# Kernel optimization log

Hardware: AMD Instinct MI355X
Metric: run time of the kernel (lower is better)

Reference implementation:

```python
import jax, jax.numpy as jnp
import numpy as np

B, H, W, CIN, COUT = 4, 128, 128, 16, 16
FH, FW = 2 * H - 1, 2 * W - 1  # fft_shape = 2*k - 1 per spatial dim (SAME, stride 1)


def setup_inputs() -> dict:
    key = jax.random.key(0)
    k1, k2, k3, k4 = jax.random.split(key, 4)
    inputs = jax.random.normal(k1, (B, H, W, CIN), dtype=jnp.float32)
    # Fourier-space complex kernel, represented as two real arrays
    kernel_real = jax.random.normal(k2, (FH, FW, CIN, COUT), dtype=jnp.float32) * 0.05
    kernel_imag = jax.random.normal(k3, (FH, FW, CIN, COUT), dtype=jnp.float32) * 0.05
    bias = jax.random.normal(k4, (1, 1, 1, COUT), dtype=jnp.float32) * 0.01
    return {"inputs": inputs, "kernel_real": kernel_real, "kernel_imag": kernel_imag, "bias": bias}


def reference(inputs, kernel_real, kernel_imag, bias):
    kernel = kernel_real + 1j * kernel_imag  # (FH, FW, CIN, COUT) complex64
    b, h, w, cin = inputs.shape
    fft_shape = (2 * h - 1, 2 * w - 1)
    # FFT over spatial dims, zero-padded to fft_shape -> (B, FH, FW, CIN) complex64
    y = jnp.fft.fftn(inputs, axes=(1, 2), s=fft_shape)
    # Broadcast complex multiply + inverse FFT: (B, FH, FW, CIN, COUT)
    y = jnp.fft.ifftn(y[..., None] * kernel, axes=(1, 2)).real
    # 'SAME' slice: center crop back to the input spatial size
    sh = (fft_shape[0] - h) // 2
    sw = (fft_shape[1] - w) // 2
    y = y[:, sh:sh + h, sw:sw + w]  # (B, H, W, CIN, COUT)
    # Faithful to the source: sum over axis=-1 (the `features` axis), leaving CIN channels
    y = jnp.sum(y, axis=-1)  # (B, H, W, CIN)
    return y + bias  # bias broadcasts because COUT == CIN
```

## Files before the change

kernel.cpp:

```cpp
#include <hip/hip_runtime.h>
#include <math.h>


constexpr float PI2_OVER_N = 6.28318530717958647692f / 255.0f;
constexpr float INV_N2 = 1.0f / (255.0f * 255.0f);

typedef __attribute__((ext_vector_type(8))) short bf16x8;
typedef __attribute__((ext_vector_type(4))) float f32x4;
#define MFMA16 __builtin_amdgcn_mfma_f32_16x16x32_bf16

__device__ __forceinline__ int remap_bc(int xidx) {
  int k = xidx & 7, j = xidx >> 3;
  return ((k >> 1) * 16) + ((k & 1) * 8) + j;
}

__device__ __forceinline__ unsigned short bf16h(float f) {
  unsigned u = __float_as_uint(f);
  return (unsigned short)((u + 0x7FFFu + ((u >> 16) & 1u)) >> 16);
}
__device__ __forceinline__ float bf16f(unsigned short h) {
  return __uint_as_float(((unsigned)h) << 16);
}


__device__ __forceinline__ void ksum_body(
    int buf, int xb, const float* __restrict__ kr, const float* __restrict__ ki,
    float* __restrict__ Sr, float* __restrict__ Si) {
  const int nrows = 255 * 255 * 16;
  int r = xb * 256 + threadIdx.x;
  if (r >= nrows) return;
  const float* src = (buf == 0) ? kr : ki;
  float* dst = (buf == 0) ? Sr : Si;
  const float4* k4 = (const float4*)(src + (size_t)r * 16);
  float4 a = k4[0], b = k4[1], c = k4[2], d = k4[3];
  dst[r] = a.x + a.y + a.z + a.w + b.x + b.y + b.z + b.w +
           c.x + c.y + c.z + c.w + d.x + d.y + d.z + d.w;
}

__device__ __forceinline__ void packx_body(
    int pid, const float* __restrict__ x, short* __restrict__ xp) {
  int bc = pid & 63;
  int mt = pid >> 6;
  int b = bc >> 4, c = bc & 15;
  int mcol = threadIdx.x & 15;
  int noct = threadIdx.x >> 4;
  int m = mt * 16 + mcol;
  const float* xs = x + ((size_t)(b * 128 + m) * 128 + noct * 8) * 16 + c;
  unsigned short hi[8], lo[8];
#pragma unroll
  for (int j = 0; j < 8; ++j) {
    float v = xs[j * 16];
    hi[j] = bf16h(v);
    lo[j] = bf16h(v - bf16f(hi[j]));
  }
  size_t base = (size_t)bc * 32768 + ((size_t)(mt * 16 + noct) * 16 + mcol) * 8;
  uint4 o;
  o.x = (unsigned)hi[0] | ((unsigned)hi[1] << 16);
  o.y = (unsigned)hi[2] | ((unsigned)hi[3] << 16);
  o.z = (unsigned)hi[4] | ((unsigned)hi[5] << 16);
  o.w = (unsigned)hi[6] | ((unsigned)hi[7] << 16);
  *(uint4*)(xp + base) = o;
  o.x = (unsigned)lo[0] | ((unsigned)lo[1] << 16);
  o.y = (unsigned)lo[2] | ((unsigned)lo[3] << 16);
  o.z = (unsigned)lo[4] | ((unsigned)lo[5] << 16);
  o.w = (unsigned)lo[6] | ((unsigned)lo[7] << 16);
  *(uint4*)(xp + base + 16384) = o;
}

__device__ __forceinline__ void buildt1_body(int cid, short* __restrict__ t1) {
  int i = cid * 256 + threadIdx.x;
  int plane = i >> 14;
  int r = i & 16383;
  int qt = r >> 11, noct = (r >> 7) & 15, qcol = (r >> 3) & 15, j = r & 7;
  int q = qt * 16 + qcol, n = noct * 8 + j;
  float s, c;
  sincosf(PI2_OVER_N * (float)((q * n) % 255), &s, &c);
  float src = (plane < 2) ? c : -s;
  unsigned short hh = bf16h(src);
  t1[i] = (short)((plane & 1) ? bf16h(src - bf16f(hh)) : hh);
}

__device__ __forceinline__ void buildt24_body(
    int cid2, short* __restrict__ t2, short* __restrict__ t4, short* __restrict__ t5) {
  int i = cid2 * 256 + threadIdx.x;
  float s, c;
  if (i < 196608) {
    int plane = i >> 15;
    int r = i & 32767;
    int pt = r >> 11, r2 = r & 2047;
    int moct = r2 >> 7, p = (r2 >> 3) & 15, j = r2 & 7;
    int pg = pt * 16 + p, m = moct * 8 + j;
    int k = ((pg % 255) * m) % 255;
    sincosf(PI2_OVER_N * (float)k, &s, &c);
    float ti = -s;
    float src = (plane < 2) ? c : ((plane < 4) ? ti : -ti);
    unsigned short h = bf16h(src);
    t2[i] = (short)((plane & 1) ? bf16h(src - bf16f(h)) : h);
  } else if (i < 393216) {
    int i2 = i - 196608;
    int plane = i2 >> 15;
    int r = i2 & 32767;
    int ht = r >> 12, r2 = r & 4095;
    int poct = r2 >> 7, h = (r2 >> 3) & 15, j = r2 & 7;
    int p = poct * 8 + j;
    unsigned short val = 0;
    if (p < 255) {
      int hg = ht * 16 + h;
      int k = ((hg + 63) * p) % 255;
      sincosf(PI2_OVER_N * (float)k, &s, &c);
      float src = (plane < 2) ? c : ((plane < 4) ? s : -s);
      unsigned short hh = bf16h(src);
      val = (plane & 1) ? bf16h(src - bf16f(hh)) : hh;
    }
    t4[i2] = (short)val;
  } else {
    int i3 = i - 393216;
    int plane = i3 >> 15;
    int r = i3 & 32767;
    int wt = r >> 12, r2 = r & 4095;
    int ko = r2 >> 7, wl = (r2 >> 3) & 15, j = r2 & 7;
    int q = (ko * 8 + j) & 127;
    int ww = wt * 16 + wl;
    sincosf(PI2_OVER_N * (float)(((ww + 63) * q) % 255), &s, &c);
    float src = (plane < 2) ? c : -s;
    unsigned short hh = bf16h(src);
    t5[i3] = (short)((plane & 1) ? bf16h(src - bf16f(hh)) : hh);
  }
}

__global__ __launch_bounds__(256) void fused_front(
    const float* __restrict__ kr, const float* __restrict__ ki,
    float* __restrict__ Sr, float* __restrict__ Si,
    const float* __restrict__ x, short* __restrict__ xp,
    short* __restrict__ t1, short* __restrict__ t2,
    short* __restrict__ t4, short* __restrict__ t5) {
  int bid = blockIdx.x;
  int d = bid >> 2, r = bid & 3;
  if (r == 3) {
    if (d < 512)      packx_body(d, x, xp);
    else if (d < 768) buildt1_body(d - 512, t1);
    else              buildt24_body(d - 768, t2, t4, t5);
  } else {
    int kid = d * 3 + r;
    if (kid < 8192) ksum_body(kid & 1, kid >> 1, kr, ki, Sr, Si);
  }
}


__device__ __forceinline__ void fold_body(
    int fid, const float* __restrict__ Sr, const float* __restrict__ Si,
    float2* __restrict__ keff2) {
  int p = fid % 255;
  int qy = fid / 255;
  int q = qy * 16 + (threadIdx.x >> 4);
  int c = threadIdx.x & 15;
  int pp = (255 - p) % 255;
  int qq = (255 - q) % 255;
  size_t i0 = (size_t)(p * 255 + q) * 16 + c;
  size_t i1 = (size_t)(pp * 255 + qq) * 16 + c;
  float sr0 = Sr[i0], si0 = Si[i0], sr1 = Sr[i1], si1 = Si[i1];
  float2 v;
  v.x = 0.5f * (sr0 + sr1);
  v.y = 0.5f * (si0 - si1);
  keff2[((size_t)c * 255 + p) * 128 + q] = v;
}

__device__ __forceinline__ void s1g_body(
    int gid, const short* __restrict__ xp, const short* __restrict__ t1,
    short* __restrict__ ub) {
  int bc = gid & 63;
  int mt = gid >> 6;
  int w = threadIdx.x >> 6;
  int lane = threadIdx.x & 63;
  int quad = lane >> 4, col = lane & 15;
  f32x4 ur[2] = {{0,0,0,0},{0,0,0,0}};
  f32x4 ui[2] = {{0,0,0,0},{0,0,0,0}};
  const short* xb = xp + (size_t)bc * 32768;
#pragma unroll
  for (int ko = 0; ko < 4; ++ko) {
    int noct = ko * 4 + quad;
    const short* pa = xb + ((size_t)(mt * 16 + noct) * 16 + col) * 8;
    bf16x8 xh = *(const bf16x8*)(pa);
    bf16x8 xl = *(const bf16x8*)(pa + 16384);
#pragma unroll
    for (int qq = 0; qq < 2; ++qq) {
      int qt = w * 2 + qq;
      const short* pb = t1 + ((size_t)(qt * 16 + noct) * 16 + col) * 8;
      bf16x8 ch = *(const bf16x8*)(pb);
      bf16x8 cl = *(const bf16x8*)(pb + 16384);
      bf16x8 nh = *(const bf16x8*)(pb + 2 * 16384);
      bf16x8 nl = *(const bf16x8*)(pb + 3 * 16384);
      ur[qq] = MFMA16(xh, ch, ur[qq], 0, 0, 0);
      ur[qq] = MFMA16(xh, cl, ur[qq], 0, 0, 0);
      ur[qq] = MFMA16(xl, ch, ur[qq], 0, 0, 0);
      ur[qq] = MFMA16(xl, cl, ur[qq], 0, 0, 0);
      ui[qq] = MFMA16(xh, nh, ui[qq], 0, 0, 0);
      ui[qq] = MFMA16(xh, nl, ui[qq], 0, 0, 0);
      ui[qq] = MFMA16(xl, nh, ui[qq], 0, 0, 0);
      ui[qq] = MFMA16(xl, nl, ui[qq], 0, 0, 0);
    }
  }
  int moct = mt * 2 + (quad >> 1);
  int j0 = (quad & 1) * 4;
#pragma unroll
  for (int qq = 0; qq < 2; ++qq) {
    int qt = w * 2 + qq;
    unsigned short rh[4], rl[4], ih[4], il[4];
#pragma unroll
    for (int r = 0; r < 4; ++r) {
      rh[r] = bf16h(ur[qq][r]); rl[r] = bf16h(ur[qq][r] - bf16f(rh[r]));
      ih[r] = bf16h(ui[qq][r]); il[r] = bf16h(ui[qq][r] - bf16f(ih[r]));
    }
    size_t base = (size_t)bc * 65536 + (size_t)qt * 2048 + (size_t)moct * 128 +
                  (size_t)col * 8 + j0;
    uint2 o;
    o.x = (unsigned)rh[0] | ((unsigned)rh[1] << 16);
    o.y = (unsigned)rh[2] | ((unsigned)rh[3] << 16);
    *(uint2*)(ub + base) = o;
    o.x = (unsigned)rl[0] | ((unsigned)rl[1] << 16);
    o.y = (unsigned)rl[2] | ((unsigned)rl[3] << 16);
    *(uint2*)(ub + base + 16384) = o;
    o.x = (unsigned)ih[0] | ((unsigned)ih[1] << 16);
    o.y = (unsigned)ih[2] | ((unsigned)ih[3] << 16);
    *(uint2*)(ub + base + 2 * 16384) = o;
    o.x = (unsigned)il[0] | ((unsigned)il[1] << 16);
    o.y = (unsigned)il[2] | ((unsigned)il[3] << 16);
    *(uint2*)(ub + base + 3 * 16384) = o;
  }
}

__global__ __launch_bounds__(256) void mid(
    const float* __restrict__ Sr, const float* __restrict__ Si,
    float2* __restrict__ keff2,
    const short* __restrict__ xp, const short* __restrict__ t1,
    short* __restrict__ ub) {
  int bid = blockIdx.x;
  int d = bid / 5, r = bid - d * 5;
  if (r == 4) {
    s1g_body(d, xp, t1, ub);
  } else {
    int fid = d * 4 + r;
    if (fid < 2040) fold_body(fid, Sr, Si, keff2);
  }
}

__global__ __launch_bounds__(256) void stage2_mfma(
    const short* __restrict__ ub, const short* __restrict__ t2,
    const float2* __restrict__ keff2, short* __restrict__ zb) {
  int bc = remap_bc(blockIdx.x);
  int c = bc & 15;
  int w = threadIdx.x >> 6;
  int lane = threadIdx.x & 63;
  int quad = lane >> 4, col = lane & 15;
  int pt = blockIdx.y;
  int qh = w;
  f32x4 accr[2] = {{0,0,0,0},{0,0,0,0}};
  f32x4 acci[2] = {{0,0,0,0},{0,0,0,0}};
  const short* ubase = ub + (size_t)bc * 65536;
#pragma unroll
  for (int ko = 0; ko < 4; ++ko) {
    int moct = ko * 4 + quad;
    const short* ta = t2 + ((size_t)(pt * 16 + moct) * 16 + col) * 8;
    bf16x8 arh = *(const bf16x8*)(ta);
    bf16x8 arl = *(const bf16x8*)(ta + 32768);
    bf16x8 aih = *(const bf16x8*)(ta + 2 * 32768);
    bf16x8 ail = *(const bf16x8*)(ta + 3 * 32768);
    bf16x8 anh = *(const bf16x8*)(ta + 4 * 32768);
    bf16x8 anl = *(const bf16x8*)(ta + 5 * 32768);
#pragma unroll
    for (int qq = 0; qq < 2; ++qq) {
      int qt = qh * 2 + qq;
      const short* tb = ubase + ((size_t)(qt * 16 + moct) * 16 + col) * 8;
      bf16x8 brh = *(const bf16x8*)(tb);
      bf16x8 brl = *(const bf16x8*)(tb + 16384);
      bf16x8 bih = *(const bf16x8*)(tb + 2 * 16384);
      bf16x8 bil = *(const bf16x8*)(tb + 3 * 16384);
      accr[qq] = MFMA16(arh, brh, accr[qq], 0, 0, 0);
      accr[qq] = MFMA16(arh, brl, accr[qq], 0, 0, 0);
      accr[qq] = MFMA16(arl, brh, accr[qq], 0, 0, 0);
      accr[qq] = MFMA16(anh, bih, accr[qq], 0, 0, 0);
      accr[qq] = MFMA16(anh, bil, accr[qq], 0, 0, 0);
      accr[qq] = MFMA16(anl, bih, accr[qq], 0, 0, 0);
      acci[qq] = MFMA16(arh, bih, acci[qq], 0, 0, 0);
      acci[qq] = MFMA16(arh, bil, acci[qq], 0, 0, 0);
      acci[qq] = MFMA16(arl, bih, acci[qq], 0, 0, 0);
      acci[qq] = MFMA16(aih, brh, acci[qq], 0, 0, 0);
      acci[qq] = MFMA16(aih, brl, acci[qq], 0, 0, 0);
      acci[qq] = MFMA16(ail, brh, acci[qq], 0, 0, 0);
    }
  }
  int poct = pt * 2 + (quad >> 1);
  size_t joff = (size_t)col * 8 + (quad & 1) * 4;
#pragma unroll
  for (int qq = 0; qq < 2; ++qq) {
    int qt = qh * 2 + qq;
    int qg = qt * 16 + col;
    float zr[4], zi[4];
#pragma unroll
    for (int r = 0; r < 4; ++r) {
      int pg = pt * 16 + quad * 4 + r;
      int pgc = pg < 255 ? pg : 254;
      float2 k = keff2[((size_t)c * 255 + pgc) * 128 + qg];
      float xr = accr[qq][r], xi = acci[qq][r];
      zr[r] = k.x * xr - k.y * xi;
      zi[r] = k.x * xi + k.y * xr;
    }
    unsigned short hr[4], lr[4], hi_[4], li[4];
#pragma unroll
    for (int r = 0; r < 4; ++r) {
      hr[r] = bf16h(zr[r]);  lr[r] = bf16h(zr[r] - bf16f(hr[r]));
      hi_[r] = bf16h(zi[r]); li[r] = bf16h(zi[r] - bf16f(hi_[r]));
    }
    size_t base = (size_t)bc * 131072 + (size_t)qt * 4096 + (size_t)poct * 128 + joff;
    uint2 o;
    o.x = (unsigned)hr[0] | ((unsigned)hr[1] << 16);
    o.y = (unsigned)hr[2] | ((unsigned)hr[3] << 16);
    *(uint2*)(zb + base) = o;
    o.x = (unsigned)lr[0] | ((unsigned)lr[1] << 16);
    o.y = (unsigned)lr[2] | ((unsigned)lr[3] << 16);
    *(uint2*)(zb + base + 32768) = o;
    o.x = (unsigned)hi_[0] | ((unsigned)hi_[1] << 16);
    o.y = (unsigned)hi_[2] | ((unsigned)hi_[3] << 16);
    *(uint2*)(zb + base + 2 * 32768) = o;
    o.x = (unsigned)li[0] | ((unsigned)li[1] << 16);
    o.y = (unsigned)li[2] | ((unsigned)li[3] << 16);
    *(uint2*)(zb + base + 3 * 32768) = o;
  }
}

__global__ __launch_bounds__(256) void stage4_mfma(
    const short* __restrict__ zb, const short* __restrict__ t4,
    short* __restrict__ a5, float* __restrict__ v0) {
  int bc = remap_bc(blockIdx.x);
  int w = threadIdx.x >> 6;
  int lane = threadIdx.x & 63;
  int quad = lane >> 4, col = lane & 15;
  int u = blockIdx.y * 4 + w;
  int qt = u >> 3;
  int kseg = (u >> 2) & 1;
  int htp = u & 3;
  f32x4 accr[2] = {{0,0,0,0},{0,0,0,0}};
  f32x4 acci[2] = {{0,0,0,0},{0,0,0,0}};
  const short* zbase = zb + (size_t)bc * 131072;
#pragma unroll
  for (int ko = 0; ko < 4; ++ko) {
    int poct = kseg * 16 + ko * 4 + quad;
    const short* tz = zbase + ((size_t)(qt * 32 + poct) * 16 + col) * 8;
    bf16x8 zrh = *(const bf16x8*)(tz);
    bf16x8 zrl = *(const bf16x8*)(tz + 32768);
    bf16x8 zih = *(const bf16x8*)(tz + 2 * 32768);
    bf16x8 zil = *(const bf16x8*)(tz + 3 * 32768);
#pragma unroll
    for (int t = 0; t < 2; ++t) {
      int ht = htp * 2 + t;
      const short* ta = t4 + ((size_t)(ht * 32 + poct) * 16 + col) * 8;
      bf16x8 trh = *(const bf16x8*)(ta);
      bf16x8 trl = *(const bf16x8*)(ta + 32768);
      bf16x8 tih = *(const bf16x8*)(ta + 2 * 32768);
      bf16x8 til = *(const bf16x8*)(ta + 3 * 32768);
      bf16x8 tnh = *(const bf16x8*)(ta + 4 * 32768);
      bf16x8 tnl = *(const bf16x8*)(ta + 5 * 32768);
      accr[t] = MFMA16(zrh, trh, accr[t], 0, 0, 0);
      accr[t] = MFMA16(zrh, trl, accr[t], 0, 0, 0);
      accr[t] = MFMA16(zrl, trh, accr[t], 0, 0, 0);
      accr[t] = MFMA16(zih, tnh, accr[t], 0, 0, 0);
      accr[t] = MFMA16(zih, tnl, accr[t], 0, 0, 0);
      accr[t] = MFMA16(zil, tnh, accr[t], 0, 0, 0);
      acci[t] = MFMA16(zih, trh, acci[t], 0, 0, 0);
      acci[t] = MFMA16(zih, trl, acci[t], 0, 0, 0);
      acci[t] = MFMA16(zil, trh, acci[t], 0, 0, 0);
      acci[t] = MFMA16(zrh, tih, acci[t], 0, 0, 0);
      acci[t] = MFMA16(zrh, til, acci[t], 0, 0, 0);
      acci[t] = MFMA16(zrl, tih, acci[t], 0, 0, 0);
    }
  }
  int ko_s = kseg * 16 + qt * 2 + (quad >> 1);
  int j0 = (quad & 1) * 4;
#pragma unroll
  for (int t = 0; t < 2; ++t) {
    int ht = htp * 2 + t;
    unsigned short vh[4], vl[4], wh[4], wl2[4];
#pragma unroll
    for (int r = 0; r < 4; ++r) {
      vh[r] = bf16h(accr[t][r]);  vl[r] = bf16h(accr[t][r] - bf16f(vh[r]));
      wh[r] = bf16h(acci[t][r]);  wl2[r] = bf16h(acci[t][r] - bf16f(wh[r]));
    }
    size_t base = (((size_t)(bc * 4) * 8 + ht) * 32 + ko_s) * 128 + (size_t)col * 8 + j0;
    uint2 o;
    o.x = (unsigned)vh[0] | ((unsigned)vh[1] << 16);
    o.y = (unsigned)vh[2] | ((unsigned)vh[3] << 16);
    *(uint2*)(a5 + base) = o;
    o.x = (unsigned)vl[0] | ((unsigned)vl[1] << 16);
    o.y = (unsigned)vl[2] | ((unsigned)vl[3] << 16);
    *(uint2*)(a5 + base + 32768) = o;
    o.x = (unsigned)wh[0] | ((unsigned)wh[1] << 16);
    o.y = (unsigned)wh[2] | ((unsigned)wh[3] << 16);
    *(uint2*)(a5 + base + 2 * 32768) = o;
    o.x = (unsigned)wl2[0] | ((unsigned)wl2[1] << 16);
    o.y = (unsigned)wl2[2] | ((unsigned)wl2[3] << 16);
    *(uint2*)(a5 + base + 3 * 32768) = o;
    if (qt == 0 && quad == 0)
      v0[(size_t)(kseg * 64 + bc) * 128 + ht * 16 + col] = accr[t][0];
  }
}

__global__ __launch_bounds__(256) void stage5_mfma(
    const short* __restrict__ a5, const short* __restrict__ t5,
    const float* __restrict__ v0, const float* __restrict__ bias,
    float* __restrict__ out) {
  int bc = remap_bc(blockIdx.x);
  int w = threadIdx.x >> 6;
  int lane = threadIdx.x & 63;
  int quad = lane >> 4, col = lane & 15;
  int u = blockIdx.y * 4 + w;
  int ht = u >> 2;
  int wtp = u & 3;
  f32x4 acc[2] = {{0,0,0,0},{0,0,0,0}};
  const short* abase = a5 + (size_t)bc * 131072;
#pragma unroll
  for (int kc = 0; kc < 8; ++kc) {
    int koq = kc * 4 + quad;
    const short* pa = abase + ((size_t)(ht * 32 + koq) * 16 + col) * 8;
    bf16x8 vrh = *(const bf16x8*)(pa);
    bf16x8 vrl = *(const bf16x8*)(pa + 32768);
    bf16x8 vih = *(const bf16x8*)(pa + 2 * 32768);
    bf16x8 vil = *(const bf16x8*)(pa + 3 * 32768);
#pragma unroll
    for (int t = 0; t < 2; ++t) {
      int wt = wtp * 2 + t;
      const short* pb = t5 + ((size_t)(wt * 32 + koq) * 16 + col) * 8;
      bf16x8 tch = *(const bf16x8*)(pb);
      bf16x8 tcl = *(const bf16x8*)(pb + 32768);
      bf16x8 tnh = *(const bf16x8*)(pb + 2 * 32768);
      bf16x8 tnl = *(const bf16x8*)(pb + 3 * 32768);
      acc[t] = MFMA16(vrh, tch, acc[t], 0, 0, 0);
      acc[t] = MFMA16(vrh, tcl, acc[t], 0, 0, 0);
      acc[t] = MFMA16(vrl, tch, acc[t], 0, 0, 0);
      acc[t] = MFMA16(vih, tnh, acc[t], 0, 0, 0);
      acc[t] = MFMA16(vih, tnl, acc[t], 0, 0, 0);
      acc[t] = MFMA16(vil, tnh, acc[t], 0, 0, 0);
    }
  }
  int b = bc >> 4, c = bc & 15;
  float bb = bias[c];
  float v0t[4];
#pragma unroll
  for (int r = 0; r < 4; ++r) {
    int h = ht * 16 + quad * 4 + r;
    v0t[r] = v0[(size_t)bc * 128 + h] + v0[(size_t)(64 + bc) * 128 + h];
  }
#pragma unroll
  for (int t = 0; t < 2; ++t) {
    int ww = (wtp * 2 + t) * 16 + col;
#pragma unroll
    for (int r = 0; r < 4; ++r) {
      int h = ht * 16 + quad * 4 + r;
      out[((size_t)(b * 128 + h) * 128 + ww) * 16 + c] =
          (2.0f * acc[t][r] - v0t[r]) * INV_N2 + bb;
    }
  }
}

extern "C" void kernel_launch(void* const* d_in, const int* in_sizes, int n_in,
                              void* d_out, int out_size, void* d_ws, size_t ws_size,
                              hipStream_t stream) {
  const float* x  = (const float*)d_in[0];
  const float* kr = (const float*)d_in[1];
  const float* ki = (const float*)d_in[2];
  const float* bs = (const float*)d_in[3];
  float* out = (float*)d_out;

  char* p = (char*)d_ws;
  float2* keff2 = (float2*)p; p += (size_t)16 * 255 * 128 * 8;
  short*  zb    = (short*)p;  p += (size_t)64 * 131072 * 2;
  char*   a5reg = p;
  short*  a5    = (short*)p;  p += (size_t)64 * 131072 * 2;
  short*  ub    = (short*)p;  p += (size_t)64 * 65536 * 2;
  short*  t2    = (short*)p;  p += (size_t)196608 * 2;
  short*  t4    = (short*)p;  p += (size_t)196608 * 2;
  short*  t5    = (short*)p;  p += (size_t)131072 * 2;
  float*  v0    = (float*)p;  p += (size_t)2 * 64 * 128 * 4;
  float* Sr = (float*)zb;
  float* Si = Sr + 255 * 255 * 16;
  short* xp = (short*)a5reg;
  short* t1 = (short*)(a5reg + 6 * 1024 * 1024);

  fused_front<<<11264, 256, 0, stream>>>(kr, ki, Sr, Si, x, xp, t1, t2, t4, t5);
  mid<<<2560, 256, 0, stream>>>(Sr, Si, keff2, xp, t1, ub);
  stage2_mfma<<<dim3(64, 16), 256, 0, stream>>>(ub, t2, keff2, zb);
  stage4_mfma<<<dim3(64, 16), 256, 0, stream>>>(zb, t4, a5, v0);
  stage5_mfma<<<dim3(64, 8), 256, 0, stream>>>(a5, t5, v0, bs, out);
}
```

Measured before the change: 208.4 us.

## Remap stage2 waves to own whole row tiles and use nontemporal kernel loads

In stage2 each wave now owns one p-tile and all eight q-tiles, rather than the four waves of a block splitting the q-tiles of a shared p-tile. The grid shrinks from 16 to 4 blocks along y. Each wave loads its A fragments once and reuses them across eight MFMA accumulator pairs, at the cost of more accumulator registers and fewer blocks in flight. The kernel-sum stage also switches its streaming float4 loads to nontemporal loads so they do not pollute the cache.

```diff
diff --git a/kernel.cpp b/kernel.cpp
--- a/kernel.cpp
+++ b/kernel.cpp
@@ -31,8 +31,11 @@
   if (r >= nrows) return;
   const float* src = (buf == 0) ? kr : ki;
   float* dst = (buf == 0) ? Sr : Si;
-  const float4* k4 = (const float4*)(src + (size_t)r * 16);
-  float4 a = k4[0], b = k4[1], c = k4[2], d = k4[3];
+  const f32x4* k4 = (const f32x4*)(src + (size_t)r * 16);
+  f32x4 a = __builtin_nontemporal_load(k4);
+  f32x4 b = __builtin_nontemporal_load(k4 + 1);
+  f32x4 c = __builtin_nontemporal_load(k4 + 2);
+  f32x4 d = __builtin_nontemporal_load(k4 + 3);
   dst[r] = a.x + a.y + a.z + a.w + b.x + b.y + b.z + b.w +
            c.x + c.y + c.z + c.w + d.x + d.y + d.z + d.w;
 }
@@ -249,13 +252,16 @@
     const float2* __restrict__ keff2, short* __restrict__ zb) {
   int bc = remap_bc(blockIdx.x);
   int c = bc & 15;
-  int w = threadIdx.x >> 6;
+  int wv = threadIdx.x >> 6;
   int lane = threadIdx.x & 63;
   int quad = lane >> 4, col = lane & 15;
-  int pt = blockIdx.y;
-  int qh = w;
-  f32x4 accr[2] = {{0,0,0,0},{0,0,0,0}};
-  f32x4 acci[2] = {{0,0,0,0},{0,0,0,0}};
+  int pt = blockIdx.y * 4 + wv;
+  f32x4 accr[8], acci[8];
+#pragma unroll
+  for (int qt = 0; qt < 8; ++qt) {
+    accr[qt] = (f32x4){0, 0, 0, 0};
+    acci[qt] = (f32x4){0, 0, 0, 0};
+  }
   const short* ubase = ub + (size_t)bc * 65536;
 #pragma unroll
   for (int ko = 0; ko < 4; ++ko) {
@@ -268,32 +274,30 @@
     bf16x8 anh = *(const bf16x8*)(ta + 4 * 32768);
     bf16x8 anl = *(const bf16x8*)(ta + 5 * 32768);
 #pragma unroll
-    for (int qq = 0; qq < 2; ++qq) {
-      int qt = qh * 2 + qq;
+    for (int qt = 0; qt < 8; ++qt) {
       const short* tb = ubase + ((size_t)(qt * 16 + moct) * 16 + col) * 8;
       bf16x8 brh = *(const bf16x8*)(tb);
       bf16x8 brl = *(const bf16x8*)(tb + 16384);
       bf16x8 bih = *(const bf16x8*)(tb + 2 * 16384);
       bf16x8 bil = *(const bf16x8*)(tb + 3 * 16384);
-      accr[qq] = MFMA16(arh, brh, accr[qq], 0, 0, 0);
-      accr[qq] = MFMA16(arh, brl, accr[qq], 0, 0, 0);
-      accr[qq] = MFMA16(arl, brh, accr[qq], 0, 0, 0);
-      accr[qq] = MFMA16(anh, bih, accr[qq], 0, 0, 0);
-      accr[qq] = MFMA16(anh, bil, accr[qq], 0, 0, 0);
-      accr[qq] = MFMA16(anl, bih, accr[qq], 0, 0, 0);
-      acci[qq] = MFMA16(arh, bih, acci[qq], 0, 0, 0);
-      acci[qq] = MFMA16(arh, bil, acci[qq], 0, 0, 0);
-      acci[qq] = MFMA16(arl, bih, acci[qq], 0, 0, 0);
-      acci[qq] = MFMA16(aih, brh, acci[qq], 0, 0, 0);
-      acci[qq] = MFMA16(aih, brl, acci[qq], 0, 0, 0);
-      acci[qq] = MFMA16(ail, brh, acci[qq], 0, 0, 0);
+      accr[qt] = MFMA16(arh, brh, accr[qt], 0, 0, 0);
+      accr[qt] = MFMA16(arh, brl, accr[qt], 0, 0, 0);
+      accr[qt] = MFMA16(arl, brh, accr[qt], 0, 0, 0);
+      accr[qt] = MFMA16(anh, bih, accr[qt], 0, 0, 0);
+      accr[qt] = MFMA16(anh, bil, accr[qt], 0, 0, 0);
+      accr[qt] = MFMA16(anl, bih, accr[qt], 0, 0, 0);
+      acci[qt] = MFMA16(arh, bih, acci[qt], 0, 0, 0);
+      acci[qt] = MFMA16(arh, bil, acci[qt], 0, 0, 0);
+      acci[qt] = MFMA16(arl, bih, acci[qt], 0, 0, 0);
+      acci[qt] = MFMA16(aih, brh, acci[qt], 0, 0, 0);
+      acci[qt] = MFMA16(aih, brl, acci[qt], 0, 0, 0);
+      acci[qt] = MFMA16(ail, brh, acci[qt], 0, 0, 0);
     }
   }
   int poct = pt * 2 + (quad >> 1);
   size_t joff = (size_t)col * 8 + (quad & 1) * 4;
 #pragma unroll
-  for (int qq = 0; qq < 2; ++qq) {
-    int qt = qh * 2 + qq;
+  for (int qt = 0; qt < 8; ++qt) {
     int qg = qt * 16 + col;
     float zr[4], zi[4];
 #pragma unroll
@@ -301,7 +305,7 @@
       int pg = pt * 16 + quad * 4 + r;
       int pgc = pg < 255 ? pg : 254;
       float2 k = keff2[((size_t)c * 255 + pgc) * 128 + qg];
-      float xr = accr[qq][r], xi = acci[qq][r];
+      float xr = accr[qt][r], xi = acci[qt][r];
       zr[r] = k.x * xr - k.y * xi;
       zi[r] = k.x * xi + k.y * xr;
     }
@@ -487,7 +491,7 @@
 
   fused_front<<<11264, 256, 0, stream>>>(kr, ki, Sr, Si, x, xp, t1, t2, t4, t5);
   mid<<<2560, 256, 0, stream>>>(Sr, Si, keff2, xp, t1, ub);
-  stage2_mfma<<<dim3(64, 16), 256, 0, stream>>>(ub, t2, keff2, zb);
+  stage2_mfma<<<dim3(64, 4), 256, 0, stream>>>(ub, t2, keff2, zb);
   stage4_mfma<<<dim3(64, 16), 256, 0, stream>>>(zb, t4, a5, v0);
   stage5_mfma<<<dim3(64, 8), 256, 0, stream>>>(a5, t5, v0, bs, out);
 }
```

After: 226.2 us. 1.09x slower.
